# Kernel optimization log

Hardware: AMD Instinct MI355X
Metric: run time of the kernel (lower is better)

Reference implementation:

```python
import jax, jax.numpy as jnp
import numpy as np

D_MODEL = 1024
STATE_DIM = 256


def setup_inputs() -> dict:
    key = jax.random.key(0)
    k_u, k_lam, k_B, k_C = jax.random.split(key, 4)
    u = jax.random.normal(k_u, (4, 4096, D_MODEL), dtype=jnp.float32)
    # log_lambda ~ N(3.0, 0.5^2), matching torch.randn(state_dim)*0.5 + 3.0
    log_lambda = jax.random.normal(k_lam, (STATE_DIM,), dtype=jnp.float32) * 0.5 + 3.0
    # torch Linear weights: B.weight [state_dim, d_model], C.weight [d_model, state_dim]
    B_w = jax.random.normal(k_B, (STATE_DIM, D_MODEL), dtype=jnp.float32) / np.sqrt(D_MODEL)
    C_w = jax.random.normal(k_C, (D_MODEL, STATE_DIM), dtype=jnp.float32) / np.sqrt(STATE_DIM)
    D = jnp.zeros((D_MODEL,), dtype=jnp.float32)
    return {"u": u, "log_lambda": log_lambda, "B_w": B_w, "C_w": C_w, "D": D}


def reference(u, log_lambda, B_w, C_w, D):
    # u: [batch, seq, d_model]
    lam = jax.nn.sigmoid(log_lambda)                      # [state_dim]
    Bu = jnp.einsum('bsd,nd->bsn', u, B_w)                # [batch, seq, state_dim]

    def step(h, bu_t):
        h = lam * h + bu_t                                # [batch, state_dim]
        return h, h

    h0 = jnp.zeros((u.shape[0], lam.shape[0]), dtype=u.dtype)
    # scan over time axis; Bu transposed to [seq, batch, state_dim]
    _, hs = jax.lax.scan(step, h0, jnp.swapaxes(Bu, 0, 1))
    hs = jnp.swapaxes(hs, 0, 1)                           # [batch, seq, state_dim]
    y = jnp.einsum('bsn,dn->bsd', hs, C_w) + D * u        # [batch, seq, d_model]
    return y
```

## Files before the change

### kernel.cpp

```cpp
#include <hip/hip_runtime.h>
#include <math.h>

typedef unsigned short ushort_t;
typedef __bf16 v8bf __attribute__((ext_vector_type(8)));
typedef __bf16 v4bf __attribute__((ext_vector_type(4)));
typedef float  v4f  __attribute__((ext_vector_type(4)));
typedef float  f32x4 __attribute__((ext_vector_type(4)));

#define BATCH 4
#define SEQ 4096
#define DM 1024
#define NS 256
#define MROWS (BATCH*SEQ)

#define NCH 128
#define CL (SEQ/NCH)

#define BK 32
#define KSPLIT 2
#define KHALF (DM/KSPLIT)

typedef __attribute__((address_space(1))) void as1_void;
typedef __attribute__((address_space(3))) void as3_void;

__device__ __forceinline__ void gl_lds16(const void* g, void* l) {
    __builtin_amdgcn_global_load_lds((as1_void*)g, (as3_void*)l, 16, 0, 0);
}

__device__ __forceinline__ ushort_t f2bf(float f) {
    unsigned u = __builtin_bit_cast(unsigned, f);
    u += 0x7fff + ((u >> 16) & 1);
    return (ushort_t)(u >> 16);
}

__device__ __forceinline__ float sigm(float x) { return 1.0f / (1.0f + expf(-x)); }

__device__ __forceinline__ float powk(int e, float l1, float l2, float l4,
                                      float l8, float l16) {
    float w = 1.0f;
    if (e & 1)  w *= l1;
    if (e & 2)  w *= l2;
    if (e & 4)  w *= l4;
    if (e & 8)  w *= l8;
    if (e & 16) w *= l16;
    return w;
}

__global__ __launch_bounds__(256)
void gemm1_fused(const float* __restrict__ A,
                 const ushort_t* __restrict__ B,
                 float* __restrict__ BuP,
                 const float* __restrict__ ll,
                 float* __restrict__ cfP)
{
    const int K = DM;
    __shared__ __align__(16) ushort_t As[2][64*BK];
    __shared__ __align__(16) ushort_t Bs[2][256*BK];

    const int tid  = threadIdx.x;
    const int lane = tid & 63;
    const int wave = tid >> 6;
    const int kidx = blockIdx.x;
    const int m0   = blockIdx.y * 64;
    const int kb   = kidx * KHALF;

    const int fr = lane & 15;
    const int fq = lane >> 4;

    int arow[2], ac4[2];
    #pragma unroll
    for (int j = 0; j < 2; ++j) {
        int cid = j*256 + tid;
        arow[j] = cid >> 3;
        ac4[j]  = (cid & 7) * 4;
    }
    int brow[4], bc[4];
    #pragma unroll
    for (int j = 0; j < 4; ++j) {
        int cid = j*256 + tid;
        brow[j] = cid >> 2;
        bc[j]   = (cid & 3) * 8;
    }

    f32x4 acc[4][4] = {};
    v4f areg[2];

    #pragma unroll
    for (int j = 0; j < 2; ++j)
        areg[j] = *(const v4f*)&A[(size_t)(m0 + arow[j])*K + kb + ac4[j]];
    #pragma unroll
    for (int j = 0; j < 4; ++j)
        gl_lds16(&B[(size_t)brow[j]*K + kb + bc[j]], &Bs[0][(j*256 + tid)*8]);

    for (int it = 0; it < KHALF/BK; ++it) {
        const int cur = it & 1;
        #pragma unroll
        for (int j = 0; j < 2; ++j)
            *(v4bf*)&As[cur][arow[j]*BK + ac4[j]] = __builtin_convertvector(areg[j], v4bf);
        __syncthreads();

        if (it + 1 < KHALF/BK) {
            const int k1 = kb + (it + 1) * BK;
            #pragma unroll
            for (int j = 0; j < 4; ++j)
                gl_lds16(&B[(size_t)brow[j]*K + k1 + bc[j]], &Bs[cur^1][(j*256 + tid)*8]);
            #pragma unroll
            for (int j = 0; j < 2; ++j)
                areg[j] = *(const v4f*)&A[(size_t)(m0 + arow[j])*K + k1 + ac4[j]];
        }

        v8bf af[4], bf[4];
        #pragma unroll
        for (int mi = 0; mi < 4; ++mi)
            af[mi] = *reinterpret_cast<const v8bf*>(&As[cur][(mi*16 + fr)*BK + fq*8]);
        #pragma unroll
        for (int ni = 0; ni < 4; ++ni)
            bf[ni] = *reinterpret_cast<const v8bf*>(&Bs[cur][(wave*64 + ni*16 + fr)*BK + fq*8]);

        #pragma unroll
        for (int mi = 0; mi < 4; ++mi)
            #pragma unroll
            for (int ni = 0; ni < 4; ++ni)
                acc[mi][ni] = __builtin_amdgcn_mfma_f32_16x16x32_bf16(
                                  af[mi], bf[ni], acc[mi][ni], 0, 0, 0);
    }

    float* Bu = BuP + (size_t)kidx*MROWS*NS;
    const int base = (lane >> 4) * 4;
    #pragma unroll
    for (int mi = 0; mi < 4; ++mi) {
        #pragma unroll
        for (int ni = 0; ni < 4; ++ni) {
            const int col = wave*64 + ni*16 + fr;
            #pragma unroll
            for (int r = 0; r < 4; ++r)
                Bu[(size_t)(m0 + mi*16 + base + r)*NS + col] = acc[mi][ni][r];
        }
    }

    const int b_idx  = m0 >> 12;
    const int c_base = (m0 & 4095) >> 5;
    float* cfk = cfP + (size_t)kidx*BATCH*NCH*NS;

    #pragma unroll
    for (int ni = 0; ni < 4; ++ni) {
        const int col = wave*64 + ni*16 + fr;
        const float l1  = sigm(ll[col]);
        const float l2  = l1*l1;
        const float l4  = l2*l2;
        const float l8  = l4*l4;
        const float l16 = l8*l8;
        #pragma unroll
        for (int h = 0; h < 2; ++h) {
            float f = 0.0f;
            #pragma unroll
            for (int mi2 = 0; mi2 < 2; ++mi2) {
                const int mi = 2*h + mi2;
                float w = powk(28 - mi2*16 - base, l1, l2, l4, l8, l16);
                f = fmaf(w, acc[mi][ni][3], f);
                w *= l1; f = fmaf(w, acc[mi][ni][2], f);
                w *= l1; f = fmaf(w, acc[mi][ni][1], f);
                w *= l1; f = fmaf(w, acc[mi][ni][0], f);
            }
            f += __shfl_xor(f, 16, 64);
            f += __shfl_xor(f, 32, 64);
            if ((lane >> 4) == 0) {
                const int chunk = c_base + h;
                cfk[((size_t)b_idx*NCH + chunk)*NS + col] = f;
            }
        }
    }
}

__global__ __launch_bounds__(256)
void gemm2_mfma(const ushort_t* __restrict__ A,
                const ushort_t* __restrict__ B,
                float* __restrict__ C,
                const float* __restrict__ Dvec, const float* __restrict__ U)
{
    const int K = NS;
    const int N = DM;
    __shared__ __align__(16) ushort_t As[2][128*BK];
    __shared__ __align__(16) ushort_t Bs[2][128*BK];

    const int tid  = threadIdx.x;
    const int lane = tid & 63;
    const int wave = tid >> 6;
    const int wrow = wave >> 1;
    const int wcol = wave & 1;
    const int n0 = blockIdx.x * 128;
    const int m0 = blockIdx.y * 128;

    const int fr = lane & 15;
    const int fq = lane >> 4;

    f32x4 acc[4][4] = {};

    const int ch0 = wave*128 + lane;
    const int ch1 = ch0 + 64;
    const int r0 = ch0 >> 2, c0 = (ch0 & 3) * 8;
    const int r1 = ch1 >> 2, c1 = (ch1 & 3) * 8;

    gl_lds16(&A[(size_t)(m0 + r0)*K + c0], &As[0][ch0*8]);
    gl_lds16(&B[(size_t)(n0 + r0)*K + c0], &Bs[0][ch0*8]);
    gl_lds16(&A[(size_t)(m0 + r1)*K + c1], &As[0][ch1*8]);
    gl_lds16(&B[(size_t)(n0 + r1)*K + c1], &Bs[0][ch1*8]);

    for (int it = 0; it < K/BK; ++it) {
        const int cur = it & 1;
        __syncthreads();

        if (it + 1 < K/BK) {
            const int k1 = (it + 1) * BK;
            gl_lds16(&A[(size_t)(m0 + r0)*K + k1 + c0], &As[cur^1][ch0*8]);
            gl_lds16(&B[(size_t)(n0 + r0)*K + k1 + c0], &Bs[cur^1][ch0*8]);
            gl_lds16(&A[(size_t)(m0 + r1)*K + k1 + c1], &As[cur^1][ch1*8]);
            gl_lds16(&B[(size_t)(n0 + r1)*K + k1 + c1], &Bs[cur^1][ch1*8]);
        }

        v8bf af[4], bf[4];
        #pragma unroll
        for (int mi = 0; mi < 4; ++mi)
            af[mi] = *reinterpret_cast<const v8bf*>(&As[cur][(wrow*64 + mi*16 + fr)*BK + fq*8]);
        #pragma unroll
        for (int ni = 0; ni < 4; ++ni)
            bf[ni] = *reinterpret_cast<const v8bf*>(&Bs[cur][(wcol*64 + ni*16 + fr)*BK + fq*8]);

        #pragma unroll
        for (int mi = 0; mi < 4; ++mi)
            #pragma unroll
            for (int ni = 0; ni < 4; ++ni)
                acc[mi][ni] = __builtin_amdgcn_mfma_f32_16x16x32_bf16(
                                  af[mi], bf[ni], acc[mi][ni], 0, 0, 0);
    }

    const int orow = m0 + wrow*64 + (lane >> 4)*4;
    const int ocol = n0 + wcol*64 + (lane & 15);
    #pragma unroll
    for (int ni = 0; ni < 4; ++ni) {
        const int col = ocol + ni*16;
        const float d = Dvec[col];
        #pragma unroll
        for (int mi = 0; mi < 4; ++mi) {
            #pragma unroll
            for (int r = 0; r < 4; ++r) {
                const size_t idx = (size_t)(orow + mi*16 + r) * N + col;
                float v = acc[mi][ni][r];
                if (d != 0.0f) v = fmaf(d, U[idx], v);
                C[idx] = v;
            }
        }
    }
}

__global__ __launch_bounds__(256)
void cvt_w(const float4* __restrict__ Bw, const float4* __restrict__ Cw,
           ushort_t* __restrict__ Bo, ushort_t* __restrict__ Co)
{
    const int i = blockIdx.x * 256 + threadIdx.x;
    const float4* src = blockIdx.y ? Cw : Bw;
    ushort_t*     dst = blockIdx.y ? Co : Bo;
    float4 v = src[i];
    ushort4 o;
    o.x = f2bf(v.x); o.y = f2bf(v.y); o.z = f2bf(v.z); o.w = f2bf(v.w);
    *(ushort4*)&dst[4*(size_t)i] = o;
}

__global__ __launch_bounds__(256)
void carry_scan(const float* __restrict__ ll, const float* __restrict__ cfP,
                float* __restrict__ carry)
{
    const int n = threadIdx.x, b = blockIdx.x;
    const float lam = sigm(ll[n]);
    float lamL = lam;
    #pragma unroll
    for (int i = 0; i < 5; ++i) lamL *= lamL;

    const float* cf0 = cfP + (size_t)b*NCH*NS + n;
    const float* cf1 = cf0 + (size_t)BATCH*NCH*NS;
    float*       cab = carry + (size_t)b*NCH*NS + n;

    float x = 0.0f;
    for (int c0 = 0; c0 < NCH; c0 += 16) {
        float v[16];
        #pragma unroll
        for (int j = 0; j < 16; ++j)
            v[j] = cf0[(size_t)(c0 + j)*NS] + cf1[(size_t)(c0 + j)*NS];
        #pragma unroll
        for (int j = 0; j < 16; ++j) {
            cab[(size_t)(c0 + j)*NS] = x;
            x = fmaf(lamL, x, v[j]);
        }
    }
}

__global__ __launch_bounds__(256)
void scan_apply(const float* __restrict__ BuP, const float* __restrict__ ll,
                const float* __restrict__ carry, ushort_t* __restrict__ hs16)
{
    const int n = threadIdx.x, c = blockIdx.x, b = blockIdx.y;
    const float lam = sigm(ll[n]);
    const size_t base = ((size_t)b*SEQ + (size_t)c*CL)*NS + n;
    const float* Bu0 = BuP;
    const float* Bu1 = BuP + (size_t)MROWS*NS;

    float v[CL];
    #pragma unroll
    for (int t = 0; t < CL; ++t)
        v[t] = Bu0[base + (size_t)t*NS] + Bu1[base + (size_t)t*NS];

    float h = carry[((size_t)b*NCH + c)*NS + n];
    #pragma unroll
    for (int t = 0; t < CL; ++t) { h = fmaf(lam, h, v[t]); v[t] = h; }
    #pragma unroll
    for (int t = 0; t < CL; ++t) hs16[base + (size_t)t*NS] = f2bf(v[t]);
}

extern "C" void kernel_launch(void* const* d_in, const int* in_sizes, int n_in,
                              void* d_out, int out_size, void* d_ws, size_t ws_size,
                              hipStream_t stream) {
    const float* u          = (const float*)d_in[0];
    const float* log_lambda = (const float*)d_in[1];
    const float* B_w        = (const float*)d_in[2];
    const float* C_w        = (const float*)d_in[3];
    const float* Dv         = (const float*)d_in[4];
    float* y  = (float*)d_out;

    char* w = (char*)d_ws;
    float*    BuP   = (float*)w;
    ushort_t* hs16  = (ushort_t*)(w + 33554432);
    ushort_t* Bw16  = (ushort_t*)(w + 41943040);
    ushort_t* Cw16  = (ushort_t*)(w + 42467328);
    float*    cfP   = (float*)(w + 42991616);
    float*    carry = (float*)(w + 44040192);

    dim3 blk(256);

    cvt_w<<<dim3(256, 2), blk, 0, stream>>>((const float4*)B_w, (const float4*)C_w,
                                            Bw16, Cw16);

    gemm1_fused<<<dim3(KSPLIT, MROWS/64), blk, 0, stream>>>(
        u, Bw16, BuP, log_lambda, cfP);

    carry_scan<<<dim3(BATCH),      blk, 0, stream>>>(log_lambda, cfP, carry);
    scan_apply<<<dim3(NCH, BATCH), blk, 0, stream>>>(BuP, log_lambda, carry, hs16);

    gemm2_mfma<<<dim3(DM/128, MROWS/128), blk, 0, stream>>>(
        hs16, Cw16, y, Dv, u);
}
```

Baseline: 175.3 us.

## Drop K-split in gemm1 and fold the carry scan into scan_apply

gemm1 now covers the full K dimension in one block of 32 rows with a BK of 64, instead of splitting K in two and writing two partial Bu buffers. This halves the Bu write and read traffic and removes the partial-sum adds. The separate single-pass carry_scan kernel is removed. Each scan_apply block instead recomputes its carry by scanning the chunk finals of all earlier chunks, which cuts one launch and its serial dependency but adds redundant work that grows with the chunk index. The gemm1 grid is now 1D with 512 blocks of 32 rows, where before it had 512 blocks of 64 rows with K split in two, so B-tile reuse per block goes down.

```diff
diff --git a/kernel.cpp b/kernel.cpp
--- a/kernel.cpp
+++ b/kernel.cpp
@@ -17,8 +17,7 @@
 #define CL (SEQ/NCH)
 
 #define BK 32
-#define KSPLIT 2
-#define KHALF (DM/KSPLIT)
+#define BK1 64
 
 typedef __attribute__((address_space(1))) void as1_void;
 typedef __attribute__((address_space(3))) void as3_void;
@@ -49,20 +48,18 @@
 __global__ __launch_bounds__(256)
 void gemm1_fused(const float* __restrict__ A,
                  const ushort_t* __restrict__ B,
-                 float* __restrict__ BuP,
+                 float* __restrict__ Bu,
                  const float* __restrict__ ll,
-                 float* __restrict__ cfP)
+                 float* __restrict__ cf)
 {
     const int K = DM;
-    __shared__ __align__(16) ushort_t As[2][64*BK];
-    __shared__ __align__(16) ushort_t Bs[2][256*BK];
+    __shared__ __align__(16) ushort_t As[2][32*BK1];
+    __shared__ __align__(16) ushort_t Bs[2][256*BK1];
 
     const int tid  = threadIdx.x;
     const int lane = tid & 63;
     const int wave = tid >> 6;
-    const int kidx = blockIdx.x;
-    const int m0   = blockIdx.y * 64;
-    const int kb   = kidx * KHALF;
+    const int m0   = blockIdx.x * 32;
 
     const int fr = lane & 15;
     const int fq = lane >> 4;
@@ -71,76 +68,79 @@
     #pragma unroll
     for (int j = 0; j < 2; ++j) {
         int cid = j*256 + tid;
-        arow[j] = cid >> 3;
-        ac4[j]  = (cid & 7) * 4;
-    }
-    int brow[4], bc[4];
-    #pragma unroll
-    for (int j = 0; j < 4; ++j) {
+        arow[j] = cid >> 4;
+        ac4[j]  = (cid & 15) * 4;
+    }
+    int brow[8], bc[8];
+    #pragma unroll
+    for (int j = 0; j < 8; ++j) {
         int cid = j*256 + tid;
-        brow[j] = cid >> 2;
-        bc[j]   = (cid & 3) * 8;
-    }
-
-    f32x4 acc[4][4] = {};
+        brow[j] = cid >> 3;
+        bc[j]   = (cid & 7) * 8;
+    }
+
+    f32x4 acc[2][4] = {};
     v4f areg[2];
 
     #pragma unroll
     for (int j = 0; j < 2; ++j)
-        areg[j] = *(const v4f*)&A[(size_t)(m0 + arow[j])*K + kb + ac4[j]];
-    #pragma unroll
-    for (int j = 0; j < 4; ++j)
-        gl_lds16(&B[(size_t)brow[j]*K + kb + bc[j]], &Bs[0][(j*256 + tid)*8]);
-
-    for (int it = 0; it < KHALF/BK; ++it) {
+        areg[j] = *(const v4f*)&A[(size_t)(m0 + arow[j])*K + ac4[j]];
+    #pragma unroll
+    for (int j = 0; j < 8; ++j)
+        gl_lds16(&B[(size_t)brow[j]*K + bc[j]], &Bs[0][(j*256 + tid)*8]);
+
+    const int NIT = K / BK1;
+    for (int it = 0; it < NIT; ++it) {
         const int cur = it & 1;
         #pragma unroll
         for (int j = 0; j < 2; ++j)
-            *(v4bf*)&As[cur][arow[j]*BK + ac4[j]] = __builtin_convertvector(areg[j], v4bf);
+            *(v4bf*)&As[cur][arow[j]*BK1 + ac4[j]] = __builtin_convertvector(areg[j], v4bf);
         __syncthreads();
 
-        if (it + 1 < KHALF/BK) {
-            const int k1 = kb + (it + 1) * BK;
-            #pragma unroll
-            for (int j = 0; j < 4; ++j)
+        if (it + 1 < NIT) {
+            const int k1 = (it + 1) * BK1;
+            #pragma unroll
+            for (int j = 0; j < 8; ++j)
                 gl_lds16(&B[(size_t)brow[j]*K + k1 + bc[j]], &Bs[cur^1][(j*256 + tid)*8]);
             #pragma unroll
             for (int j = 0; j < 2; ++j)
                 areg[j] = *(const v4f*)&A[(size_t)(m0 + arow[j])*K + k1 + ac4[j]];
         }
 
-        v8bf af[4], bf[4];
-        #pragma unroll
-        for (int mi = 0; mi < 4; ++mi)
-            af[mi] = *reinterpret_cast<const v8bf*>(&As[cur][(mi*16 + fr)*BK + fq*8]);
-        #pragma unroll
-        for (int ni = 0; ni < 4; ++ni)
-            bf[ni] = *reinterpret_cast<const v8bf*>(&Bs[cur][(wave*64 + ni*16 + fr)*BK + fq*8]);
-
-        #pragma unroll
-        for (int mi = 0; mi < 4; ++mi)
+        #pragma unroll
+        for (int kk = 0; kk < 2; ++kk) {
+            v8bf af[2], bf[4];
+            #pragma unroll
+            for (int mi = 0; mi < 2; ++mi)
+                af[mi] = *reinterpret_cast<const v8bf*>(
+                    &As[cur][(mi*16 + fr)*BK1 + kk*32 + fq*8]);
             #pragma unroll
             for (int ni = 0; ni < 4; ++ni)
-                acc[mi][ni] = __builtin_amdgcn_mfma_f32_16x16x32_bf16(
-                                  af[mi], bf[ni], acc[mi][ni], 0, 0, 0);
-    }
-
-    float* Bu = BuP + (size_t)kidx*MROWS*NS;
-    const int base = (lane >> 4) * 4;
-    #pragma unroll
-    for (int mi = 0; mi < 4; ++mi) {
+                bf[ni] = *reinterpret_cast<const v8bf*>(
+                    &Bs[cur][(wave*64 + ni*16 + fr)*BK1 + kk*32 + fq*8]);
+
+            #pragma unroll
+            for (int mi = 0; mi < 2; ++mi)
+                #pragma unroll
+                for (int ni = 0; ni < 4; ++ni)
+                    acc[mi][ni] = __builtin_amdgcn_mfma_f32_16x16x32_bf16(
+                                      af[mi], bf[ni], acc[mi][ni], 0, 0, 0);
+        }
+    }
+
+    #pragma unroll
+    for (int mi = 0; mi < 2; ++mi) {
         #pragma unroll
         for (int ni = 0; ni < 4; ++ni) {
             const int col = wave*64 + ni*16 + fr;
             #pragma unroll
             for (int r = 0; r < 4; ++r)
-                Bu[(size_t)(m0 + mi*16 + base + r)*NS + col] = acc[mi][ni][r];
-        }
-    }
-
-    const int b_idx  = m0 >> 12;
-    const int c_base = (m0 & 4095) >> 5;
-    float* cfk = cfP + (size_t)kidx*BATCH*NCH*NS;
+                Bu[(size_t)(m0 + mi*16 + fq*4 + r)*NS + col] = acc[mi][ni][r];
+        }
+    }
+
+    const int b_idx = m0 >> 12;
+    const int c_idx = (m0 & 4095) >> 5;
 
     #pragma unroll
     for (int ni = 0; ni < 4; ++ni) {
@@ -150,25 +150,19 @@
         const float l4  = l2*l2;
         const float l8  = l4*l4;
         const float l16 = l8*l8;
-        #pragma unroll
-        for (int h = 0; h < 2; ++h) {
-            float f = 0.0f;
-            #pragma unroll
-            for (int mi2 = 0; mi2 < 2; ++mi2) {
-                const int mi = 2*h + mi2;
-                float w = powk(28 - mi2*16 - base, l1, l2, l4, l8, l16);
-                f = fmaf(w, acc[mi][ni][3], f);
-                w *= l1; f = fmaf(w, acc[mi][ni][2], f);
-                w *= l1; f = fmaf(w, acc[mi][ni][1], f);
-                w *= l1; f = fmaf(w, acc[mi][ni][0], f);
-            }
-            f += __shfl_xor(f, 16, 64);
-            f += __shfl_xor(f, 32, 64);
-            if ((lane >> 4) == 0) {
-                const int chunk = c_base + h;
-                cfk[((size_t)b_idx*NCH + chunk)*NS + col] = f;
-            }
-        }
+        float f = 0.0f;
+        #pragma unroll
+        for (int mi = 0; mi < 2; ++mi) {
+            float w = powk(28 - mi*16 - fq*4, l1, l2, l4, l8, l16);
+            f = fmaf(w, acc[mi][ni][3], f);
+            w *= l1; f = fmaf(w, acc[mi][ni][2], f);
+            w *= l1; f = fmaf(w, acc[mi][ni][1], f);
+            w *= l1; f = fmaf(w, acc[mi][ni][0], f);
+        }
+        f += __shfl_xor(f, 16, 64);
+        f += __shfl_xor(f, 32, 64);
+        if (fq == 0)
+            cf[((size_t)b_idx*NCH + c_idx)*NS + col] = f;
     }
 }
 
@@ -267,49 +261,37 @@
 }
 
 __global__ __launch_bounds__(256)
-void carry_scan(const float* __restrict__ ll, const float* __restrict__ cfP,
-                float* __restrict__ carry)
-{
-    const int n = threadIdx.x, b = blockIdx.x;
-    const float lam = sigm(ll[n]);
-    float lamL = lam;
-    #pragma unroll
-    for (int i = 0; i < 5; ++i) lamL *= lamL;
-
-    const float* cf0 = cfP + (size_t)b*NCH*NS + n;
-    const float* cf1 = cf0 + (size_t)BATCH*NCH*NS;
-    float*       cab = carry + (size_t)b*NCH*NS + n;
-
-    float x = 0.0f;
-    for (int c0 = 0; c0 < NCH; c0 += 16) {
-        float v[16];
-        #pragma unroll
-        for (int j = 0; j < 16; ++j)
-            v[j] = cf0[(size_t)(c0 + j)*NS] + cf1[(size_t)(c0 + j)*NS];
-        #pragma unroll
-        for (int j = 0; j < 16; ++j) {
-            cab[(size_t)(c0 + j)*NS] = x;
-            x = fmaf(lamL, x, v[j]);
-        }
-    }
-}
-
-__global__ __launch_bounds__(256)
-void scan_apply(const float* __restrict__ BuP, const float* __restrict__ ll,
-                const float* __restrict__ carry, ushort_t* __restrict__ hs16)
+void scan_apply(const float* __restrict__ Bu, const float* __restrict__ ll,
+                const float* __restrict__ cf, ushort_t* __restrict__ hs16)
 {
     const int n = threadIdx.x, c = blockIdx.x, b = blockIdx.y;
     const float lam = sigm(ll[n]);
+    float lamL = lam;
+    #pragma unroll
+    for (int i = 0; i < 5; ++i) lamL *= lamL;
+
+    const float* cfb = cf + (size_t)b*NCH*NS + n;
+    float x = 0.0f;
+    for (int c0 = 0; c0 < c; c0 += 16) {
+        float v[16];
+        #pragma unroll
+        for (int j = 0; j < 16; ++j) {
+            const int cc = c0 + j;
+            v[j] = (cc < c) ? cfb[(size_t)cc*NS] : 0.0f;
+        }
+        #pragma unroll
+        for (int j = 0; j < 16; ++j) {
+            if (c0 + j < c) x = fmaf(lamL, x, v[j]);
+        }
+    }
+
     const size_t base = ((size_t)b*SEQ + (size_t)c*CL)*NS + n;
-    const float* Bu0 = BuP;
-    const float* Bu1 = BuP + (size_t)MROWS*NS;
-
     float v[CL];
     #pragma unroll
     for (int t = 0; t < CL; ++t)
-        v[t] = Bu0[base + (size_t)t*NS] + Bu1[base + (size_t)t*NS];
-
-    float h = carry[((size_t)b*NCH + c)*NS + n];
+        v[t] = Bu[base + (size_t)t*NS];
+
+    float h = x;
     #pragma unroll
     for (int t = 0; t < CL; ++t) { h = fmaf(lam, h, v[t]); v[t] = h; }
     #pragma unroll
@@ -327,23 +309,20 @@
     float* y  = (float*)d_out;
 
     char* w = (char*)d_ws;
-    float*    BuP   = (float*)w;
-    ushort_t* hs16  = (ushort_t*)(w + 33554432);
-    ushort_t* Bw16  = (ushort_t*)(w + 41943040);
-    ushort_t* Cw16  = (ushort_t*)(w + 42467328);
-    float*    cfP   = (float*)(w + 42991616);
-    float*    carry = (float*)(w + 44040192);
+    float*    Bu    = (float*)w;
+    ushort_t* hs16  = (ushort_t*)(w + 16777216);
+    ushort_t* Bw16  = (ushort_t*)(w + 25165824);
+    ushort_t* Cw16  = (ushort_t*)(w + 25690112);
+    float*    cf    = (float*)(w + 26214400);
 
     dim3 blk(256);
 
     cvt_w<<<dim3(256, 2), blk, 0, stream>>>((const float4*)B_w, (const float4*)C_w,
                                             Bw16, Cw16);
 
-    gemm1_fused<<<dim3(KSPLIT, MROWS/64), blk, 0, stream>>>(
-        u, Bw16, BuP, log_lambda, cfP);
-
-    carry_scan<<<dim3(BATCH),      blk, 0, stream>>>(log_lambda, cfP, carry);
-    scan_apply<<<dim3(NCH, BATCH), blk, 0, stream>>>(BuP, log_lambda, carry, hs16);
+    gemm1_fused<<<dim3(MROWS/32), blk, 0, stream>>>(u, Bw16, Bu, log_lambda, cf);
+
+    scan_apply<<<dim3(NCH, BATCH), blk, 0, stream>>>(Bu, log_lambda, cf, hs16);
 
     gemm2_mfma<<<dim3(DM/128, MROWS/128), blk, 0, stream>>>(
         hs16, Cw16, y, Dv, u);
```

Result: faster. 167.8 us (-4.3%).
